# Performance work log

Hardware: AMD Instinct MI355X
Metric: run time of the kernel (lower is better)

## Reference

```python
import jax, jax.numpy as jnp
import numpy as np

NEG_INF = -9e15  # matches the torch -9000000000000000.0 mask value
LRELU_SLOPE = 0.01  # torch nn.LeakyReLU default


def setup_inputs() -> dict:
    key = jax.random.key(0)
    k1, k2, k3, k4 = jax.random.split(key, 4)
    N, F_in, F_out = 8192, 256, 128
    x = jax.random.normal(k1, (N, F_in), dtype=jnp.float32)
    adj = jax.random.randint(k2, (N, N), 0, 2, dtype=jnp.int32)
    # xavier_uniform with gain=1.414
    limW = 1.414 * np.sqrt(6.0 / (F_in + F_out))
    W = jax.random.uniform(k3, (F_in, F_out), minval=-limW, maxval=limW, dtype=jnp.float32)
    lima = 1.414 * np.sqrt(6.0 / (2 * F_out + 1))
    a = jax.random.uniform(k4, (2 * F_out, 1), minval=-lima, maxval=lima, dtype=jnp.float32)
    return {"x": x, "adj": adj, "W": W, "a": a}


def reference(x, adj, W, a):
    # h: [N, F_out]
    h = x @ W
    F_out = h.shape[1]
    a1 = a[:F_out, 0]   # attention vector for source node i
    a2 = a[F_out:, 0]   # attention vector for target node j
    # e[i, j] = leaky_relu(h_i . a1 + h_j . a2) -- equivalent to the repeat/cat
    # construction without materializing the [N, N, 2F] tensor.
    e = (h @ a1)[:, None] + (h @ a2)[None, :]  # [N, N]
    e = jnp.where(e > 0, e, LRELU_SLOPE * e)
    scores = jnp.where(adj > 0, e, NEG_INF)
    attention = jax.nn.softmax(scores, axis=1)  # dropout omitted (eval mode)
    h_prime = attention @ h  # [N, F_out]
    return jax.nn.elu(h_prime)
```

## Files before the change

### kernel.cpp

```cpp
#include <hip/hip_runtime.h>
#include <hip/hip_bf16.h>
#include <stdint.h>


#define N_NODES 8192
#define F_INF   256
#define F_OUT   128
#define LRELU   0.01f

typedef __bf16 bf16x8 __attribute__((ext_vector_type(8)));
typedef float  f32x4  __attribute__((ext_vector_type(4)));
using bf16 = __hip_bfloat16;

__device__ __forceinline__ float b2f(bf16 v) { return __bfloat162float(v); }
__device__ __forceinline__ bf16  f2b(float v) { return __float2bfloat16(v); }

__global__ __launch_bounds__(256) void k_wa(const float* __restrict__ W,
                                            const float* __restrict__ a,
                                            float* __restrict__ wa) {
    const int k = threadIdx.x;
    const float* wr = W + (size_t)k * F_OUT;
    float v1 = 0.f, v2 = 0.f;
    for (int f = 0; f < F_OUT; ++f) {
        float w = wr[f];
        v1 += w * a[f];
        v2 += w * a[F_OUT + f];
    }
    wa[k] = v1;
    wa[F_INF + k] = v2;
}

__global__ __launch_bounds__(256) void k_xw(const float* __restrict__ x,
                                            const float* __restrict__ W,
                                            bf16* __restrict__ hT) {
    __shared__ __align__(16) bf16 WT[F_OUT][F_INF + 8];
    __shared__ __align__(16) bf16 XS[64][72];
    const int tid  = threadIdx.x;
    const int lane = tid & 63, wave = tid >> 6;
    const int i0   = blockIdx.x * 64;
    for (int idx = tid; idx < (F_INF * F_OUT) / 8; idx += 256) {
        int k  = idx >> 4;
        int n0 = (idx & 15) * 8;
        const float* src = W + (size_t)k * F_OUT + n0;
        float4 va = *(const float4*)(src);
        float4 vb = *(const float4*)(src + 4);
        float v[8] = {va.x, va.y, va.z, va.w, vb.x, vb.y, vb.z, vb.w};
#pragma unroll
        for (int c = 0; c < 8; ++c) WT[n0 + c][k] = f2b(v[c]);
    }
    __syncthreads();
    f32x4 acc[8];
#pragma unroll
    for (int t = 0; t < 8; ++t) acc[t] = {0.f, 0.f, 0.f, 0.f};
    const int m = lane & 15, quad = lane >> 4;
    const int rt = wave;
    for (int kc = 0; kc < F_INF / 64; ++kc) {
        const int k0 = kc * 64;
        {
            int part = tid & 7;
            int r    = tid >> 3;
#pragma unroll
            for (int p = 0; p < 2; ++p) {
                int rr = r + p * 32;
                const float* src = x + (size_t)(i0 + rr) * F_INF + k0 + part * 8;
                float4 va = *(const float4*)(src);
                float4 vb = *(const float4*)(src + 4);
                float v[8] = {va.x, va.y, va.z, va.w, vb.x, vb.y, vb.z, vb.w};
                __align__(16) bf16 th[8];
#pragma unroll
                for (int c = 0; c < 8; ++c) th[c] = f2b(v[c]);
                *(uint4*)(&XS[rr][part * 8]) = *(const uint4*)th;
            }
        }
        __syncthreads();
#pragma unroll
        for (int ks = 0; ks < 2; ++ks) {
            bf16x8 af = *(const bf16x8*)(&XS[rt * 16 + m][ks * 32 + quad * 8]);
#pragma unroll
            for (int ct = 0; ct < 8; ++ct) {
                bf16x8 bfr = *(const bf16x8*)(&WT[ct * 16 + m][k0 + ks * 32 + quad * 8]);
                acc[ct] = __builtin_amdgcn_mfma_f32_16x16x32_bf16(af, bfr, acc[ct], 0, 0, 0);
            }
        }
        __syncthreads();
    }
#pragma unroll
    for (int ct = 0; ct < 8; ++ct) {
        const int f = ct * 16 + m;
#pragma unroll
        for (int r = 0; r < 4; ++r) {
            const int i = i0 + rt * 16 + quad * 4 + r;
            hT[(size_t)f * N_NODES + i] = f2b(acc[ct][r]);
        }
    }
}

__global__ __launch_bounds__(256) void k_s12(const float* __restrict__ x,
                                             const float* __restrict__ wa,
                                             float* __restrict__ s1,
                                             float* __restrict__ s2) {
    const int tid  = threadIdx.x;
    const int lane = tid & 63, wave = tid >> 6;
    float4 w1 = *(const float4*)(wa + lane * 4);
    float4 w2 = *(const float4*)(wa + F_INF + lane * 4);
    const int ibase = (blockIdx.x * 4 + wave) * 64;
    for (int r = 0; r < 64; ++r) {
        const int i = ibase + r;
        float4 xv = *(const float4*)(x + (size_t)i * F_INF + lane * 4);
        float v1 = xv.x * w1.x + xv.y * w1.y + xv.z * w1.z + xv.w * w1.w;
        float v2 = xv.x * w2.x + xv.y * w2.y + xv.z * w2.z + xv.w * w2.w;
#pragma unroll
        for (int off = 32; off >= 1; off >>= 1) {
            v1 += __shfl_xor(v1, off);
            v2 += __shfl_xor(v2, off);
        }
        if (lane == 0) { s1[i] = v1; s2[i] = v2; }
    }
}

__global__ __launch_bounds__(256) void k_max(const float* __restrict__ s2,
                                             float* __restrict__ mg) {
    __shared__ float red[256];
    int tid = threadIdx.x;
    float m = -1e30f;
    for (int j = tid; j < N_NODES; j += 256) m = fmaxf(m, s2[j]);
    red[tid] = m;
    __syncthreads();
    for (int s = 128; s > 0; s >>= 1) {
        if (tid < s) red[tid] = fmaxf(red[tid], red[tid + s]);
        __syncthreads();
    }
    if (tid == 0) mg[0] = red[0];
}

__global__ __launch_bounds__(256, 4) void k_attn(const int* __restrict__ adj,
                                                 const float* __restrict__ s1g,
                                                 const float* __restrict__ s2g,
                                                 const float* __restrict__ mg,
                                                 const bf16* __restrict__ hT,
                                                 float* __restrict__ Of,
                                                 float* __restrict__ lp) {
    __shared__ __align__(16) bf16 HS[F_OUT][72];
    __shared__ float s2s[1024];
    const int tid  = threadIdx.x;
    const int lane = tid & 63, wave = tid >> 6;
    const int m = lane & 15, quad = lane >> 4;
    const int i0    = blockIdx.x * 64;
    const int jq    = blockIdx.y;
    const int jbase = jq * 1024;
    const int irow  = i0 + wave * 16 + m;
    const float s1v = s1g[irow];
    const float tmi = s1v + mg[0];
    const float mi  = fmaxf(tmi, LRELU * tmi);
    *(float4*)&s2s[tid * 4] = *(const float4*)(s2g + jbase + tid * 4);
    const int part = tid & 7, fr = tid >> 3;
    const bf16* hTp = hT + jbase + part * 8;
    {
        uint4 v0 = *(const uint4*)(hTp + (size_t)(fr +  0) * N_NODES);
        uint4 v1 = *(const uint4*)(hTp + (size_t)(fr + 32) * N_NODES);
        uint4 v2 = *(const uint4*)(hTp + (size_t)(fr + 64) * N_NODES);
        uint4 v3 = *(const uint4*)(hTp + (size_t)(fr + 96) * N_NODES);
        *(uint4*)&HS[fr +  0][part * 8] = v0;
        *(uint4*)&HS[fr + 32][part * 8] = v1;
        *(uint4*)&HS[fr + 64][part * 8] = v2;
        *(uint4*)&HS[fr + 96][part * 8] = v3;
    }
    const int4* arowp = (const int4*)(adj + (size_t)irow * N_NODES + jbase);
    int4 av[4];
    av[0] = arowp[quad * 2];     av[1] = arowp[quad * 2 + 1];
    av[2] = arowp[8 + quad * 2]; av[3] = arowp[8 + quad * 2 + 1];
    float lacc = 0.f;
    f32x4 acc[8];
#pragma unroll
    for (int c = 0; c < 8; ++c) acc[c] = {0.f, 0.f, 0.f, 0.f};
    __syncthreads();

    for (int jc = 0; jc < 16; ++jc) {
        const int jn = (jc < 15) ? jc + 1 : 15;
        uint4 h0 = *(const uint4*)(hTp + (size_t)(fr +  0) * N_NODES + jn * 64);
        uint4 h1 = *(const uint4*)(hTp + (size_t)(fr + 32) * N_NODES + jn * 64);
        uint4 h2 = *(const uint4*)(hTp + (size_t)(fr + 64) * N_NODES + jn * 64);
        uint4 h3 = *(const uint4*)(hTp + (size_t)(fr + 96) * N_NODES + jn * 64);
        bf16x8 afrag[2];
#pragma unroll
        for (int kh = 0; kh < 2; ++kh) {
            const int am[8] = {av[kh*2].x, av[kh*2].y, av[kh*2].z, av[kh*2].w,
                               av[kh*2+1].x, av[kh*2+1].y, av[kh*2+1].z, av[kh*2+1].w};
            const float* s2p = &s2s[jc * 64 + kh * 32 + quad * 8];
            __align__(16) bf16 a8[8];
#pragma unroll
            for (int t = 0; t < 8; ++t) {
                float e = s1v + s2p[t];
                e = fmaxf(e, LRELU * e);
                float w = (am[t] > 0) ? __expf(e - mi) : 0.f;
                bf16 b = f2b(w);
                a8[t] = b;
                lacc += b2f(b);
            }
            afrag[kh] = *(const bf16x8*)a8;
        }
        av[0] = arowp[jn * 16 + quad * 2];     av[1] = arowp[jn * 16 + quad * 2 + 1];
        av[2] = arowp[jn * 16 + 8 + quad * 2]; av[3] = arowp[jn * 16 + 8 + quad * 2 + 1];
#pragma unroll
        for (int kh = 0; kh < 2; ++kh)
#pragma unroll
            for (int c = 0; c < 8; ++c) {
                bf16x8 bfr = *(const bf16x8*)(&HS[c * 16 + m][kh * 32 + quad * 8]);
                acc[c] = __builtin_amdgcn_mfma_f32_16x16x32_bf16(afrag[kh], bfr, acc[c], 0, 0, 0);
            }
        __syncthreads();
        *(uint4*)&HS[fr +  0][part * 8] = h0;
        *(uint4*)&HS[fr + 32][part * 8] = h1;
        *(uint4*)&HS[fr + 64][part * 8] = h2;
        *(uint4*)&HS[fr + 96][part * 8] = h3;
        __syncthreads();
    }
    lacc += __shfl_xor(lacc, 16);
    lacc += __shfl_xor(lacc, 32);
    if (quad == 0) lp[(size_t)jq * N_NODES + irow] = lacc;
#pragma unroll
    for (int c = 0; c < 8; ++c) {
        const int f = c * 16 + m;
#pragma unroll
        for (int r = 0; r < 4; ++r) {
            const int i = i0 + wave * 16 + quad * 4 + r;
            Of[((size_t)jq * N_NODES + i) * F_OUT + f] = acc[c][r];
        }
    }
}

__global__ __launch_bounds__(256) void k_comb(const float* __restrict__ Of,
                                              const float* __restrict__ lp,
                                              float* __restrict__ out) {
    size_t gid = (size_t)blockIdx.x * 256 + threadIdx.x;
    int i = (int)(gid >> 7);
    float s = 0.f, l = 0.f;
#pragma unroll
    for (int q = 0; q < 8; ++q) {
        s += Of[(size_t)q * (N_NODES * (size_t)F_OUT) + gid];
        l += lp[q * N_NODES + i];
    }
    float o = s / l;
    out[gid] = o > 0.f ? o : __expf(o) - 1.f;
}

extern "C" void kernel_launch(void* const* d_in, const int* in_sizes, int n_in,
                              void* d_out, int out_size, void* d_ws, size_t ws_size,
                              hipStream_t stream) {
    (void)out_size; (void)ws_size;
    const float* x   = nullptr;
    const int*   adj = nullptr;
    const float* W   = nullptr;
    const float* a   = nullptr;
    for (int ii = 0; ii < n_in; ++ii) {
        int sz = in_sizes[ii];
        if      (sz == N_NODES * F_INF)  x   = (const float*)d_in[ii];
        else if (sz == F_INF * F_OUT)    W   = (const float*)d_in[ii];
        else if (sz == 2 * F_OUT)        a   = (const float*)d_in[ii];
        else                             adj = (const int*)d_in[ii];
    }
    float* out = (float*)d_out;

    char* ws = (char*)d_ws;
    bf16*  hT = (bf16*)ws;  ws += (size_t)F_OUT * N_NODES * 2;
    float* wa = (float*)ws; ws += 2 * F_INF * 4;
    float* s1 = (float*)ws; ws += N_NODES * 4;
    float* s2 = (float*)ws; ws += N_NODES * 4;
    float* mg = (float*)ws; ws += 256;
    float* lp = (float*)ws; ws += 8 * N_NODES * 4;
    float* Of = (float*)ws;

    k_wa  <<<1, 256, 0, stream>>>(W, a, wa);
    k_xw  <<<N_NODES / 64, 256, 0, stream>>>(x, W, hT);
    k_s12 <<<N_NODES / 256, 256, 0, stream>>>(x, wa, s1, s2);
    k_max <<<1, 256, 0, stream>>>(s2, mg);
    k_attn<<<dim3(N_NODES / 64, 8), 256, 0, stream>>>(adj, s1, s2, mg, hT, Of, lp);
    k_comb<<<(N_NODES * F_OUT) / 256, 256, 0, stream>>>(Of, lp, out);
}
```

Before: 482.1 us.

## Fuse score projections into XW kernel and double-buffer H tiles in attention

Result: faster. 467.7 us (-3.0%).

```diff
diff --git a/kernel.cpp b/kernel.cpp
--- a/kernel.cpp
+++ b/kernel.cpp
@@ -15,29 +15,22 @@
 __device__ __forceinline__ float b2f(bf16 v) { return __bfloat162float(v); }
 __device__ __forceinline__ bf16  f2b(float v) { return __float2bfloat16(v); }
 
-__global__ __launch_bounds__(256) void k_wa(const float* __restrict__ W,
-                                            const float* __restrict__ a,
-                                            float* __restrict__ wa) {
-    const int k = threadIdx.x;
-    const float* wr = W + (size_t)k * F_OUT;
-    float v1 = 0.f, v2 = 0.f;
-    for (int f = 0; f < F_OUT; ++f) {
-        float w = wr[f];
-        v1 += w * a[f];
-        v2 += w * a[F_OUT + f];
-    }
-    wa[k] = v1;
-    wa[F_INF + k] = v2;
-}
-
 __global__ __launch_bounds__(256) void k_xw(const float* __restrict__ x,
                                             const float* __restrict__ W,
-                                            bf16* __restrict__ hT) {
+                                            const float* __restrict__ a,
+                                            bf16* __restrict__ hT,
+                                            float* __restrict__ s1,
+                                            float* __restrict__ s2) {
     __shared__ __align__(16) bf16 WT[F_OUT][F_INF + 8];
     __shared__ __align__(16) bf16 XS[64][72];
+    __shared__ float waL[2 * F_INF];
+    __shared__ float s1L[64], s2L[64];
     const int tid  = threadIdx.x;
     const int lane = tid & 63, wave = tid >> 6;
     const int i0   = blockIdx.x * 64;
+    waL[tid] = 0.f; waL[F_INF + tid] = 0.f;
+    if (tid < 64) { s1L[tid] = 0.f; s2L[tid] = 0.f; }
+    __syncthreads();
     for (int idx = tid; idx < (F_INF * F_OUT) / 8; idx += 256) {
         int k  = idx >> 4;
         int n0 = (idx & 15) * 8;
@@ -45,8 +38,15 @@
         float4 va = *(const float4*)(src);
         float4 vb = *(const float4*)(src + 4);
         float v[8] = {va.x, va.y, va.z, va.w, vb.x, vb.y, vb.z, vb.w};
-#pragma unroll
-        for (int c = 0; c < 8; ++c) WT[n0 + c][k] = f2b(v[c]);
+        float p1 = 0.f, p2 = 0.f;
+#pragma unroll
+        for (int c = 0; c < 8; ++c) {
+            WT[n0 + c][k] = f2b(v[c]);
+            p1 += v[c] * a[n0 + c];
+            p2 += v[c] * a[F_OUT + n0 + c];
+        }
+        atomicAdd(&waL[k], p1);
+        atomicAdd(&waL[F_INF + k], p2);
     }
     __syncthreads();
     f32x4 acc[8];
@@ -67,9 +67,16 @@
                 float4 vb = *(const float4*)(src + 4);
                 float v[8] = {va.x, va.y, va.z, va.w, vb.x, vb.y, vb.z, vb.w};
                 __align__(16) bf16 th[8];
-#pragma unroll
-                for (int c = 0; c < 8; ++c) th[c] = f2b(v[c]);
+                float q1 = 0.f, q2 = 0.f;
+#pragma unroll
+                for (int c = 0; c < 8; ++c) {
+                    th[c] = f2b(v[c]);
+                    q1 += v[c] * waL[k0 + part * 8 + c];
+                    q2 += v[c] * waL[F_INF + k0 + part * 8 + c];
+                }
                 *(uint4*)(&XS[rr][part * 8]) = *(const uint4*)th;
+                atomicAdd(&s1L[rr], q1);
+                atomicAdd(&s2L[rr], q2);
             }
         }
         __syncthreads();
@@ -78,7 +85,7 @@
             bf16x8 af = *(const bf16x8*)(&XS[rt * 16 + m][ks * 32 + quad * 8]);
 #pragma unroll
             for (int ct = 0; ct < 8; ++ct) {
-                bf16x8 bfr = *(const bf16x8*)(&WT[ct * 16 + m][k0 + ks * 32 + quad * 8]);
+                bf16x8 bfr = *(const bf16x8*)(&WT[ct * 16 + m][kc * 64 + ks * 32 + quad * 8]);
                 acc[ct] = __builtin_amdgcn_mfma_f32_16x16x32_bf16(af, bfr, acc[ct], 0, 0, 0);
             }
         }
@@ -93,29 +100,7 @@
             hT[(size_t)f * N_NODES + i] = f2b(acc[ct][r]);
         }
     }
-}
-
-__global__ __launch_bounds__(256) void k_s12(const float* __restrict__ x,
-                                             const float* __restrict__ wa,
-                                             float* __restrict__ s1,
-                                             float* __restrict__ s2) {
-    const int tid  = threadIdx.x;
-    const int lane = tid & 63, wave = tid >> 6;
-    float4 w1 = *(const float4*)(wa + lane * 4);
-    float4 w2 = *(const float4*)(wa + F_INF + lane * 4);
-    const int ibase = (blockIdx.x * 4 + wave) * 64;
-    for (int r = 0; r < 64; ++r) {
-        const int i = ibase + r;
-        float4 xv = *(const float4*)(x + (size_t)i * F_INF + lane * 4);
-        float v1 = xv.x * w1.x + xv.y * w1.y + xv.z * w1.z + xv.w * w1.w;
-        float v2 = xv.x * w2.x + xv.y * w2.y + xv.z * w2.z + xv.w * w2.w;
-#pragma unroll
-        for (int off = 32; off >= 1; off >>= 1) {
-            v1 += __shfl_xor(v1, off);
-            v2 += __shfl_xor(v2, off);
-        }
-        if (lane == 0) { s1[i] = v1; s2[i] = v2; }
-    }
+    if (tid < 64) { s1[i0 + tid] = s1L[tid]; s2[i0 + tid] = s2L[tid]; }
 }
 
 __global__ __launch_bounds__(256) void k_max(const float* __restrict__ s2,
@@ -133,14 +118,14 @@
     if (tid == 0) mg[0] = red[0];
 }
 
-__global__ __launch_bounds__(256, 4) void k_attn(const int* __restrict__ adj,
-                                                 const float* __restrict__ s1g,
-                                                 const float* __restrict__ s2g,
-                                                 const float* __restrict__ mg,
-                                                 const bf16* __restrict__ hT,
-                                                 float* __restrict__ Of,
-                                                 float* __restrict__ lp) {
-    __shared__ __align__(16) bf16 HS[F_OUT][72];
+__global__ __launch_bounds__(256) void k_attn(const int* __restrict__ adj,
+                                              const float* __restrict__ s1g,
+                                              const float* __restrict__ s2g,
+                                              const float* __restrict__ mg,
+                                              const bf16* __restrict__ hT,
+                                              float* __restrict__ Of,
+                                              float* __restrict__ lp) {
+    __shared__ __align__(16) bf16 HS[2][F_OUT][72];
     __shared__ float s2s[1024];
     const int tid  = threadIdx.x;
     const int lane = tid & 63, wave = tid >> 6;
@@ -160,32 +145,40 @@
         uint4 v1 = *(const uint4*)(hTp + (size_t)(fr + 32) * N_NODES);
         uint4 v2 = *(const uint4*)(hTp + (size_t)(fr + 64) * N_NODES);
         uint4 v3 = *(const uint4*)(hTp + (size_t)(fr + 96) * N_NODES);
-        *(uint4*)&HS[fr +  0][part * 8] = v0;
-        *(uint4*)&HS[fr + 32][part * 8] = v1;
-        *(uint4*)&HS[fr + 64][part * 8] = v2;
-        *(uint4*)&HS[fr + 96][part * 8] = v3;
-    }
+        *(uint4*)&HS[0][fr +  0][part * 8] = v0;
+        *(uint4*)&HS[0][fr + 32][part * 8] = v1;
+        *(uint4*)&HS[0][fr + 64][part * 8] = v2;
+        *(uint4*)&HS[0][fr + 96][part * 8] = v3;
+    }
+    uint4 h0 = *(const uint4*)(hTp + (size_t)(fr +  0) * N_NODES + 64);
+    uint4 h1 = *(const uint4*)(hTp + (size_t)(fr + 32) * N_NODES + 64);
+    uint4 h2 = *(const uint4*)(hTp + (size_t)(fr + 64) * N_NODES + 64);
+    uint4 h3 = *(const uint4*)(hTp + (size_t)(fr + 96) * N_NODES + 64);
     const int4* arowp = (const int4*)(adj + (size_t)irow * N_NODES + jbase);
-    int4 av[4];
-    av[0] = arowp[quad * 2];     av[1] = arowp[quad * 2 + 1];
-    av[2] = arowp[8 + quad * 2]; av[3] = arowp[8 + quad * 2 + 1];
+    int4 avA[4], avB[4];
+    avA[0] = arowp[quad * 2];          avA[1] = arowp[quad * 2 + 1];
+    avA[2] = arowp[8 + quad * 2];      avA[3] = arowp[8 + quad * 2 + 1];
+    avB[0] = arowp[16 + quad * 2];     avB[1] = arowp[16 + quad * 2 + 1];
+    avB[2] = arowp[16 + 8 + quad * 2]; avB[3] = arowp[16 + 8 + quad * 2 + 1];
     float lacc = 0.f;
     f32x4 acc[8];
 #pragma unroll
     for (int c = 0; c < 8; ++c) acc[c] = {0.f, 0.f, 0.f, 0.f};
     __syncthreads();
+    int b = 0;
 
     for (int jc = 0; jc < 16; ++jc) {
-        const int jn = (jc < 15) ? jc + 1 : 15;
-        uint4 h0 = *(const uint4*)(hTp + (size_t)(fr +  0) * N_NODES + jn * 64);
-        uint4 h1 = *(const uint4*)(hTp + (size_t)(fr + 32) * N_NODES + jn * 64);
-        uint4 h2 = *(const uint4*)(hTp + (size_t)(fr + 64) * N_NODES + jn * 64);
-        uint4 h3 = *(const uint4*)(hTp + (size_t)(fr + 96) * N_NODES + jn * 64);
+        if (jc < 15) {
+            *(uint4*)&HS[b ^ 1][fr +  0][part * 8] = h0;
+            *(uint4*)&HS[b ^ 1][fr + 32][part * 8] = h1;
+            *(uint4*)&HS[b ^ 1][fr + 64][part * 8] = h2;
+            *(uint4*)&HS[b ^ 1][fr + 96][part * 8] = h3;
+        }
         bf16x8 afrag[2];
 #pragma unroll
         for (int kh = 0; kh < 2; ++kh) {
-            const int am[8] = {av[kh*2].x, av[kh*2].y, av[kh*2].z, av[kh*2].w,
-                               av[kh*2+1].x, av[kh*2+1].y, av[kh*2+1].z, av[kh*2+1].w};
+            const int am[8] = {avA[kh*2].x, avA[kh*2].y, avA[kh*2].z, avA[kh*2].w,
+                               avA[kh*2+1].x, avA[kh*2+1].y, avA[kh*2+1].z, avA[kh*2+1].w};
             const float* s2p = &s2s[jc * 64 + kh * 32 + quad * 8];
             __align__(16) bf16 a8[8];
 #pragma unroll
@@ -193,27 +186,35 @@
                 float e = s1v + s2p[t];
                 e = fmaxf(e, LRELU * e);
                 float w = (am[t] > 0) ? __expf(e - mi) : 0.f;
-                bf16 b = f2b(w);
-                a8[t] = b;
-                lacc += b2f(b);
+                bf16 bb = f2b(w);
+                a8[t] = bb;
+                lacc += b2f(bb);
             }
             afrag[kh] = *(const bf16x8*)a8;
         }
-        av[0] = arowp[jn * 16 + quad * 2];     av[1] = arowp[jn * 16 + quad * 2 + 1];
-        av[2] = arowp[jn * 16 + 8 + quad * 2]; av[3] = arowp[jn * 16 + 8 + quad * 2 + 1];
+#pragma unroll
+        for (int q = 0; q < 4; ++q) avA[q] = avB[q];
+        if (jc < 14) {
+            const int base = (jc + 2) * 16;
+            avB[0] = arowp[base + quad * 2];     avB[1] = arowp[base + quad * 2 + 1];
+            avB[2] = arowp[base + 8 + quad * 2]; avB[3] = arowp[base + 8 + quad * 2 + 1];
+        }
+        if (jc < 14) {
+            const int off = (jc + 2) * 64;
+            h0 = *(const uint4*)(hTp + (size_t)(fr +  0) * N_NODES + off);
+            h1 = *(const uint4*)(hTp + (size_t)(fr + 32) * N_NODES + off);
+            h2 = *(const uint4*)(hTp + (size_t)(fr + 64) * N_NODES + off);
+            h3 = *(const uint4*)(hTp + (size_t)(fr + 96) * N_NODES + off);
+        }
 #pragma unroll
         for (int kh = 0; kh < 2; ++kh)
 #pragma unroll
             for (int c = 0; c < 8; ++c) {
-                bf16x8 bfr = *(const bf16x8*)(&HS[c * 16 + m][kh * 32 + quad * 8]);
+                bf16x8 bfr = *(const bf16x8*)(&HS[b][c * 16 + m][kh * 32 + quad * 8]);
                 acc[c] = __builtin_amdgcn_mfma_f32_16x16x32_bf16(afrag[kh], bfr, acc[c], 0, 0, 0);
             }
         __syncthreads();
-        *(uint4*)&HS[fr +  0][part * 8] = h0;
-        *(uint4*)&HS[fr + 32][part * 8] = h1;
-        *(uint4*)&HS[fr + 64][part * 8] = h2;
-        *(uint4*)&HS[fr + 96][part * 8] = h3;
-        __syncthreads();
+        b ^= 1;
     }
     lacc += __shfl_xor(lacc, 16);
     lacc += __shfl_xor(lacc, 32);
@@ -263,16 +264,13 @@
 
     char* ws = (char*)d_ws;
     bf16*  hT = (bf16*)ws;  ws += (size_t)F_OUT * N_NODES * 2;
-    float* wa = (float*)ws; ws += 2 * F_INF * 4;
     float* s1 = (float*)ws; ws += N_NODES * 4;
     float* s2 = (float*)ws; ws += N_NODES * 4;
     float* mg = (float*)ws; ws += 256;
     float* lp = (float*)ws; ws += 8 * N_NODES * 4;
     float* Of = (float*)ws;
 
-    k_wa  <<<1, 256, 0, stream>>>(W, a, wa);
-    k_xw  <<<N_NODES / 64, 256, 0, stream>>>(x, W, hT);
-    k_s12 <<<N_NODES / 256, 256, 0, stream>>>(x, wa, s1, s2);
+    k_xw  <<<N_NODES / 64, 256, 0, stream>>>(x, W, a, hT, s1, s2);
     k_max <<<1, 256, 0, stream>>>(s2, mg);
     k_attn<<<dim3(N_NODES / 64, 8), 256, 0, stream>>>(adj, s1, s2, mg, hT, Of, lp);
     k_comb<<<(N_NODES * F_OUT) / 256, 256, 0, stream>>>(Of, lp, out);
```
